# Optimization experiments

Hardware: AMD Instinct MI355X
Metric: run time of the kernel (lower is better)

Reference implementation:

```python
import jax, jax.numpy as jnp
import numpy as np

N_NODES = 50000
N_EDGES = 1600000
DIM = 32
N_STEPS = 10   # torchdiffeq rk4 with step_size=0.1 over t in [0, 1]
H = 0.1


def setup_inputs() -> dict:
    key = jax.random.key(0)
    ks = jax.random.split(key, 10)
    x = jax.random.normal(ks[0], (N_NODES, DIM), dtype=jnp.float32)
    pos_edge_index = jax.random.randint(ks[1], (2, N_EDGES), 0, N_NODES, dtype=jnp.int64)
    neg_edge_index = jax.random.randint(ks[2], (2, N_EDGES), 0, N_NODES, dtype=jnp.int64)
    s = 1.0 / np.sqrt(DIM)
    W_pos = jax.random.normal(ks[3], (DIM, DIM), dtype=jnp.float32) * s
    b_pos = jnp.zeros((DIM,), dtype=jnp.float32)
    wt_pos = jax.random.normal(ks[4], (DIM,), dtype=jnp.float32)
    W_neg = jax.random.normal(ks[5], (DIM, DIM), dtype=jnp.float32) * s
    b_neg = jnp.zeros((DIM,), dtype=jnp.float32)
    wt_neg = jax.random.normal(ks[6], (DIM,), dtype=jnp.float32)
    return {"x": x, "pos_edge_index": pos_edge_index, "neg_edge_index": neg_edge_index,
            "W_pos": W_pos, "b_pos": b_pos, "wt_pos": wt_pos,
            "W_neg": W_neg, "b_neg": b_neg, "wt_neg": wt_neg}


def _gcn_ode(x0, edge_index, W, b, wt):
    # PyG GCNConv with self-loops + symmetric normalization, wrapped in
    # psi(t, x) = relu(GCN(x)) * sigmoid(t * wt), integrated with RK4.
    src, dst = edge_index[0], edge_index[1]
    n = x0.shape[0]
    deg = jnp.zeros((n,), dtype=x0.dtype).at[dst].add(1.0) + 1.0  # self-loop
    dis = jax.lax.rsqrt(deg)
    edge_norm = (dis[src] * dis[dst])[:, None]   # [E,1]
    self_norm = (dis * dis)[:, None]             # [N,1] = 1/deg

    def f(t, x):
        xw = x @ W                               # [N,D]
        agg = jax.ops.segment_sum(edge_norm * xw[src], dst, num_segments=n)
        agg = agg + self_norm * xw + b
        gate = jax.nn.sigmoid(t * wt)            # [D]
        return jax.nn.relu(agg) * gate

    def step(x, t):
        k1 = f(t, x)
        k2 = f(t + H / 2, x + (H / 2) * k1)
        k3 = f(t + H / 2, x + (H / 2) * k2)
        k4 = f(t + H, x + H * k3)
        return x + (H / 6) * (k1 + 2 * k2 + 2 * k3 + k4), None

    ts = jnp.arange(N_STEPS, dtype=x0.dtype) * H
    xT, _ = jax.lax.scan(step, x0, ts)
    return xT


def reference(x, pos_edge_index, neg_edge_index, W_pos, b_pos, wt_pos, W_neg, b_neg, wt_neg):
    z_pos = _gcn_ode(x, pos_edge_index, W_pos, b_pos, wt_pos)
    z_neg = _gcn_ode(x, neg_edge_index, W_neg, b_neg, wt_neg)
    return (z_pos, z_neg)
```

## Files before the change

kernel.cpp:

```cpp
#include <hip/hip_runtime.h>

#define NN 50000
#define NE 1600000
#define DIM 32
#define HS 0.1f
#define NBPS 782
#define NEB4 1563
#define NNB 196
#define NSC 49
#define SBIN 256
#define NBIN 196
#define AB 391
#define WCAP 22528

static inline int cdiv(int a, int b) { return (a + b - 1) / b; }

typedef unsigned short ushort_t;
typedef unsigned v4u __attribute__((ext_vector_type(4)));


__device__ __forceinline__ float4 bf4_to_f4(uint2 u) {
    float4 v;
    v.x = __uint_as_float(u.x << 16);
    v.y = __uint_as_float(u.x & 0xffff0000u);
    v.z = __uint_as_float(u.y << 16);
    v.w = __uint_as_float(u.y & 0xffff0000u);
    return v;
}
__device__ __forceinline__ unsigned pack_bf2(float a, float b) {
    unsigned ua = __float_as_uint(a);
    ua = (ua + 0x7fffu + ((ua >> 16) & 1u)) >> 16;
    unsigned ub = __float_as_uint(b);
    ub = (ub + 0x7fffu + ((ub >> 16) & 1u)) & 0xffff0000u;
    return ua | ub;
}
__device__ __forceinline__ uint4 pack_bf8(float4 a, float4 b) {
    return make_uint4(pack_bf2(a.x, a.y), pack_bf2(a.z, a.w),
                      pack_bf2(b.x, b.y), pack_bf2(b.z, b.w));
}


__global__ void k_zero2(int* __restrict__ p0, int* __restrict__ p1) {
    int b = blockIdx.x, sg = b & 1;
    int i = (b >> 1) * 256 + (int)threadIdx.x;
    int* p = sg ? p1 : p0;
    if (i < NN) p[i] = 0;
}

__global__ void k_zbins(int* __restrict__ bins) {
    bins[blockIdx.x * 256 + threadIdx.x] = 0;
}

__global__ void k_hist4(const int* __restrict__ dst, int* __restrict__ cnt) {
    int base = (blockIdx.x * 256 + (int)threadIdx.x) * 4;
    if (base < NE) {
        v4u d = *(const v4u*)(dst + base);
        atomicAdd(&cnt[d.x], 1);
        atomicAdd(&cnt[d.y], 1);
        atomicAdd(&cnt[d.z], 1);
        atomicAdd(&cnt[d.w], 1);
    }
}

__global__ void k_dhist2(const int* __restrict__ c0,
                         const int* __restrict__ c1, int* __restrict__ bins) {
    __shared__ int lb[256];
    int b = blockIdx.x, sg = b & 1;
    int t = threadIdx.x;
    lb[t] = 0;
    __syncthreads();
    int n = (b >> 1) * 256 + t;
    if (n < NN) {
        const int* cnt = sg ? c1 : c0;
        int d = cnt[n]; if (d > 255) d = 255;
        atomicAdd(&lb[d], 1);
    }
    __syncthreads();
    int v = lb[t];
    if (v) atomicAdd(&bins[sg * 256 + t], v);
}

__global__ void k_dscan(int* __restrict__ bins) {
    __shared__ int s[256];
    int sg = blockIdx.x, t = threadIdx.x;
    s[t] = bins[sg * 256 + (255 - t)];
    __syncthreads();
    for (int off = 1; off < 256; off <<= 1) {
        int a = (t >= off) ? s[t - off] : 0;
        __syncthreads();
        s[t] += a;
        __syncthreads();
    }
    int ex = (t == 0) ? 0 : s[t - 1];
    bins[sg * 256 + (255 - t)] = ex;
}

__global__ void k_dperm2(const int* __restrict__ c0,
                         const int* __restrict__ c1, int* __restrict__ bins,
                         int* __restrict__ perm0, int* __restrict__ perm1,
                         int* __restrict__ pos0, int* __restrict__ pos1,
                         float* __restrict__ q0, float* __restrict__ q1) {
    __shared__ int lb[256];
    int b = blockIdx.x, sg = b & 1;
    int t = threadIdx.x;
    lb[t] = 0;
    __syncthreads();
    int n = (b >> 1) * 256 + t;
    const int* cnt = sg ? c1 : c0;
    int d = 0, lr = 0;
    if (n < NN) {
        d = cnt[n]; if (d > 255) d = 255;
        lr = atomicAdd(&lb[d], 1);
    }
    __syncthreads();
    int v = lb[t];
    __syncthreads();
    int base = 0;
    if (v) base = atomicAdd(&bins[sg * 256 + t], v);
    lb[t] = base;
    __syncthreads();
    if (n < NN) {
        int p = lb[d] + lr;
        int* perm = sg ? perm1 : perm0;
        int* pos  = sg ? pos1 : pos0;
        float* dq = sg ? q1 : q0;
        perm[p] = n;
        pos[n] = p;
        dq[p] = rsqrtf((float)cnt[n] + 1.0f);
    }
}

__global__ __launch_bounds__(1024) void k_scanA2(const int* __restrict__ c0,
                                                 const int* __restrict__ c1,
                                                 const int* __restrict__ perm0,
                                                 const int* __restrict__ perm1,
                                                 int* __restrict__ r0,
                                                 int* __restrict__ r1,
                                                 int* __restrict__ p0,
                                                 int* __restrict__ p1) {
    int sg = blockIdx.x >= NSC;
    int bb = blockIdx.x - (sg ? NSC : 0);
    const int* cnt  = sg ? c1 : c0;
    const int* perm = sg ? perm1 : perm0;
    int* row_ptr    = sg ? r1 : r0;
    int* partials   = sg ? p1 : p0;
    __shared__ int s[1024];
    int t = threadIdx.x;
    int g = bb * 1024 + t;
    int v = (g < NN) ? ((cnt[perm[g]] + 7) & ~7) : 0;
    s[t] = v;
    __syncthreads();
    for (int off = 1; off < 1024; off <<= 1) {
        int add = (t >= off) ? s[t - off] : 0;
        __syncthreads();
        s[t] += add;
        __syncthreads();
    }
    if (g < NN) row_ptr[g + 1] = s[t];
    if (t == 1023) partials[bb] = s[t];
}

__global__ void k_scanB2(int* __restrict__ p0, int* __restrict__ p1) {
    int* partials = blockIdx.x ? p1 : p0;
    if (threadIdx.x == 0) {
        int run = 0;
        for (int i = 0; i < NSC; i++) { int v = partials[i]; partials[i] = run; run += v; }
    }
}

__global__ void k_scanC2(int* __restrict__ r0, int* __restrict__ r1,
                         const int* __restrict__ p0, const int* __restrict__ p1) {
    int b = blockIdx.x, sg = b & 1;
    int g = (b >> 1) * 256 + (int)threadIdx.x;
    int* row_ptr = sg ? r1 : r0;
    const int* partials = sg ? p1 : p0;
    if (g < NN) row_ptr[g + 1] += partials[g >> 10];
    if (g == 0) row_ptr[0] = 0;
}


__global__ __launch_bounds__(512) void k_countA(const int* __restrict__ d0,
                        const int* __restrict__ d1,
                        const int* __restrict__ pos0, const int* __restrict__ pos1,
                        int* __restrict__ gc0, int* __restrict__ gc1) {
    __shared__ int lc[NBIN];
    int b = blockIdx.x, sg = b & 1, blk = b >> 1;
    int t = threadIdx.x;
    if (t < NBIN) lc[t] = 0;
    __syncthreads();
    const int* dst = sg ? d1 : d0;
    const int* pos = sg ? pos1 : pos0;
#pragma unroll
    for (int i = 0; i < 8; i++) {
        int e = blk * 4096 + i * 512 + t;
        if (e < NE) atomicAdd(&lc[pos[dst[e]] >> 8], 1);
    }
    __syncthreads();
    int* gc = sg ? gc1 : gc0;
    if (t < NBIN) gc[blk * NBIN + t] = lc[t];
}

__global__ __launch_bounds__(512) void k_scanM1(int* __restrict__ gc0,
                                                int* __restrict__ gc1,
                                                int* __restrict__ bint) {
    __shared__ int s[512];
    int b = blockIdx.x, sg = b & 1, bin = b >> 1;
    int* gc = sg ? gc1 : gc0;
    int t = threadIdx.x;
    int v = (t < AB) ? gc[t * NBIN + bin] : 0;
    s[t] = v;
    __syncthreads();
    for (int off = 1; off < 512; off <<= 1) {
        int a = (t >= off) ? s[t - off] : 0;
        __syncthreads();
        s[t] += a;
        __syncthreads();
    }
    if (t < AB) gc[t * NBIN + bin] = s[t] - v;
    if (t == AB - 1) bint[sg * NBIN + bin] = s[t];
}

__global__ __launch_bounds__(256) void k_scanM2(const int* __restrict__ bint,
                                                int* __restrict__ binbase) {
    __shared__ int s[256];
    int t = threadIdx.x;
    for (int sg = 0; sg < 2; sg++) {
        int v = (t < NBIN) ? bint[sg * NBIN + t] : 0;
        s[t] = v;
        __syncthreads();
        for (int off = 1; off < 256; off <<= 1) {
            int a = (t >= off) ? s[t - off] : 0;
            __syncthreads();
            s[t] += a;
            __syncthreads();
        }
        if (t < NBIN) binbase[sg * NBIN + t] = s[t] - v;
        __syncthreads();
    }
}

__global__ __launch_bounds__(512) void k_scatA(const int* __restrict__ s0s,
                        const int* __restrict__ s0d,
                        const int* __restrict__ s1s, const int* __restrict__ s1d,
                        const int* __restrict__ pos0, const int* __restrict__ pos1,
                        const int* __restrict__ gc0, const int* __restrict__ gc1,
                        const int* __restrict__ binbase,
                        unsigned* __restrict__ gst0, unsigned* __restrict__ gst1) {
    __shared__ int lc[NBIN];
    __shared__ int lst[NBIN];
    __shared__ int gch[NBIN];
    __shared__ unsigned stag[4096];
    __shared__ ushort_t bos[4096];
    int b = blockIdx.x, sg = b & 1, blk = b >> 1;
    int t = threadIdx.x;
    if (t < NBIN) lc[t] = 0;
    __syncthreads();
    const int* src = sg ? s1s : s0s;
    const int* dst = sg ? s1d : s0d;
    const int* pos = sg ? pos1 : pos0;
    const int* gc  = sg ? gc1 : gc0;
    unsigned er[8]; int ebin[8]; int erk[8];
#pragma unroll
    for (int i = 0; i < 8; i++) {
        int e = blk * 4096 + i * 512 + t;
        ebin[i] = -1;
        if (e < NE) {
            int pd = pos[dst[e]];
            int ps = pos[src[e]];
            int bin = pd >> 8;
            ebin[i] = bin;
            er[i] = ((unsigned)ps << 8) | (unsigned)(pd & 255);
            erk[i] = atomicAdd(&lc[bin], 1);
        }
    }
    __syncthreads();
    if (t < NBIN) lst[t] = lc[t];
    __syncthreads();
    for (int off = 1; off < NBIN; off <<= 1) {
        int a = (t >= off && t < NBIN) ? lst[t - off] : 0;
        __syncthreads();
        if (t < NBIN) lst[t] += a;
        __syncthreads();
    }
    if (t < NBIN) {
        lst[t] -= lc[t];
        gch[t] = binbase[sg * NBIN + t] + gc[blk * NBIN + t];
    }
    __syncthreads();
#pragma unroll
    for (int i = 0; i < 8; i++) {
        if (ebin[i] >= 0) {
            int slot = lst[ebin[i]] + erk[i];
            stag[slot] = er[i];
            bos[slot] = (ushort_t)ebin[i];
        }
    }
    __syncthreads();
    unsigned* gst = sg ? gst1 : gst0;
    int tot = (blk * 4096 + 4096 <= NE) ? 4096 : (NE - blk * 4096);
#pragma unroll
    for (int i = 0; i < 8; i++) {
        int slot = i * 512 + t;
        if (slot < tot) {
            int bin = bos[slot];
            gst[gch[bin] + (slot - lst[bin])] = stag[slot];
        }
    }
}

__global__ __launch_bounds__(512) void k_scatB(const int* __restrict__ r0,
                        const int* __restrict__ r1,
                        const unsigned* __restrict__ gst0,
                        const unsigned* __restrict__ gst1,
                        const int* __restrict__ bint, const int* __restrict__ binbase,
                        ushort_t* __restrict__ w0, ushort_t* __restrict__ w1) {
    __shared__ uint4 winq[WCAP / 8];
    __shared__ int lrp[SBIN + 1];
    __shared__ int lfill[SBIN];
    ushort_t* win = (ushort_t*)winq;
    int b = blockIdx.x, sg = b & 1, bin = b >> 1;
    int t = threadIdx.x;
    const int* rp = sg ? r1 : r0;
    const unsigned* gst = sg ? gst1 : gst0;
    ushort_t* cw = sg ? w1 : w0;
    int p0 = bin * SBIN;
    int nn = NN - p0; if (nn > SBIN) nn = SBIN;
    if (t <= nn) lrp[t] = rp[p0 + t];
    if (t < nn) lfill[t] = 0;
    __syncthreads();
    int wb = lrp[0];
    int wl = lrp[nn] - wb;
    int cnt = bint[sg * NBIN + bin];
    int base = binbase[sg * NBIN + bin];
    if (wl <= WCAP) {
        for (int i = t; i < cnt; i += 512) {
            unsigned e = gst[base + i];
            int pdl = e & 255u;
            int ofs = atomicAdd(&lfill[pdl], 1);
            win[lrp[pdl] - wb + ofs] = (ushort_t)(e >> 8);
        }
        __syncthreads();
        for (int ln = t; ln < nn; ln += 512) {
            int e0 = lrp[ln] - wb + lfill[ln], e1 = lrp[ln + 1] - wb;
            for (int j = e0; j < e1; j++) win[j] = (ushort_t)NN;
        }
        __syncthreads();
        uint4* dst4 = (uint4*)(cw + wb);
        int nq = wl >> 3;
        for (int i = t; i < nq; i += 512) dst4[i] = winq[i];
    } else {
        for (int i = t; i < cnt; i += 512) {
            unsigned e = gst[base + i];
            int pdl = e & 255u;
            int ofs = atomicAdd(&lfill[pdl], 1);
            cw[lrp[pdl] + ofs] = (ushort_t)(e >> 8);
        }
        __syncthreads();
        for (int ln = t; ln < nn; ln += 512) {
            int e0 = lrp[ln] + lfill[ln], e1 = lrp[ln + 1];
            for (int j = e0; j < e1; j++) cw[j] = (ushort_t)NN;
        }
    }
}

struct ZArgs { unsigned* p[6]; };
__global__ void k_zrow(ZArgs z) {
    int t = threadIdx.x;
    if (t < 96) z.p[t >> 4][(size_t)NN * 16 + (t & 15)] = 0u;
}

__global__ __launch_bounds__(256) void k_matmul(const float* __restrict__ src,
                                                const float* __restrict__ W,
                                                const int* __restrict__ cnt,
                                                const int* __restrict__ pos,
                                                uint2* __restrict__ xw,
                                                float* __restrict__ copy_out) {
    __shared__ float sW[DIM * DIM];
    __shared__ float sX[32 * 33];
    int t = threadIdx.x;
#pragma unroll
    for (int k = 0; k < 4; k++) { int i = k * 256 + t; sW[i] = W[i]; }
    size_t base = (size_t)blockIdx.x * 32 * DIM;
#pragma unroll
    for (int k = 0; k < 4; k++) {
        int i = k * 256 + t;
        size_t g = base + i;
        float v = 0.f;
        if (g < (size_t)NN * DIM) {
            v = src[g];
            copy_out[g] = v;
        }
        sX[(i >> 5) * 33 + (i & 31)] = v;
    }
    __syncthreads();
    int r = t >> 3, oct = t & 7;
    int row = blockIdx.x * 32 + r;
    if (row >= NN) return;
    float a0 = 0.f, a1 = 0.f, a2 = 0.f, a3 = 0.f;
    const float* xr = &sX[r * 33];
#pragma unroll
    for (int i = 0; i < DIM; i++) {
        float xv = xr[i];
        const float* wr = &sW[i * DIM + oct * 4];
        a0 = fmaf(xv, wr[0], a0);
        a1 = fmaf(xv, wr[1], a1);
        a2 = fmaf(xv, wr[2], a2);
        a3 = fmaf(xv, wr[3], a3);
    }
    float dn = rsqrtf((float)cnt[row] + 1.0f);
    a0 *= dn; a1 *= dn; a2 *= dn; a3 *= dn;
    xw[(size_t)pos[row] * 8 + oct] = make_uint2(pack_bf2(a0, a1), pack_bf2(a2, a3));
}


struct SignP {
    const int* row_ptr; const ushort_t* cw; const float* dis;
    const int* perm;
    const uint4* xw_in; uint4* xw_out; const uint4* xw_base;
    uint4* acc;
    float* x_cur;
    const float* W; const float* b; const float* wt;
    float* zout;
};
struct StageArgs { SignP s[2]; float t, stage_coef; int mode; };

#define EDGE_ADD(u)                                                     \
    {                                                                   \
        float4 vA = bf4_to_f4(make_uint2((u).x, (u).y));                \
        float4 vB = bf4_to_f4(make_uint2((u).z, (u).w));                \
        sum0.x += vA.x; sum0.y += vA.y; sum0.z += vA.z; sum0.w += vA.w; \
        sum1.x += vB.x; sum1.y += vB.y; sum1.z += vB.z; sum1.w += vB.w; \
    }

__global__ __launch_bounds__(256) void k_stage(StageArgs A) {
    int sg = blockIdx.x & 1;
    int blk = blockIdx.x >> 1;
    SignP P = A.s[sg];

    __shared__ float sW[DIM * DIM];
    __shared__ float sR[64 * 36];
    int tid = threadIdx.x;
    int mode = A.mode;
    if (mode != 5) {
#pragma unroll
        for (int k = 0; k < 4; k++) { int i = k * 256 + tid; sW[i] = P.W[i]; }
    }

    int c = tid & 3;
    int nl = tid >> 2;
    int n = blk * 64 + nl;
    bool active = n < NN;
    float dn = 0.f;
    float4 r40 = make_float4(0.f, 0.f, 0.f, 0.f);
    float4 r41 = make_float4(0.f, 0.f, 0.f, 0.f);
    float4 bs0 = make_float4(0.f, 0.f, 0.f, 0.f);
    float4 bs1 = make_float4(0.f, 0.f, 0.f, 0.f);

    if (active) {
        int e = P.row_ptr[n], e1 = P.row_ptr[n + 1];
        const uint4* xwq = P.xw_in + c;
        const uint4* cw4 = (const uint4*)P.cw;
        int q = e >> 3, qe = e1 >> 3;
        float4 sum0 = make_float4(0.f, 0.f, 0.f, 0.f);
        float4 sum1 = make_float4(0.f, 0.f, 0.f, 0.f);
        uint4 ra;
        if (q < qe) ra = cw4[q];
        while (q < qe) {
            unsigned s0 = ra.x & 0xffffu, s1 = ra.x >> 16;
            unsigned s2 = ra.y & 0xffffu, s3 = ra.y >> 16;
            unsigned s4 = ra.z & 0xffffu, s5 = ra.z >> 16;
            unsigned s6 = ra.w & 0xffffu, s7 = ra.w >> 16;
            uint4 u0 = xwq[(size_t)s0 * 4];
            uint4 u1 = xwq[(size_t)s1 * 4];
            uint4 u2 = xwq[(size_t)s2 * 4];
            uint4 u3 = xwq[(size_t)s3 * 4];
            uint4 u4 = xwq[(size_t)s4 * 4];
            uint4 u5 = xwq[(size_t)s5 * 4];
            uint4 u6 = xwq[(size_t)s6 * 4];
            uint4 u7 = xwq[(size_t)s7 * 4];
            int qn = q + 1;
            uint4 nx;
            if (qn < qe) nx = cw4[qn];
            EDGE_ADD(u0) EDGE_ADD(u1) EDGE_ADD(u2) EDGE_ADD(u3)
            EDGE_ADD(u4) EDGE_ADD(u5) EDGE_ADD(u6) EDGE_ADD(u7)
            if (qn < qe) ra = nx;
            q = qn;
        }
        dn = P.dis[n];
        uint4 un = xwq[(size_t)n * 4];
        float4 vn0 = bf4_to_f4(make_uint2(un.x, un.y));
        float4 vn1 = bf4_to_f4(make_uint2(un.z, un.w));
        float4 bb0 = *(const float4*)&P.b[c * 8];
        float4 bb1 = *(const float4*)&P.b[c * 8 + 4];
        sum0.x = fmaf(dn, sum0.x + vn0.x, bb0.x);
        sum0.y = fmaf(dn, sum0.y + vn0.y, bb0.y);
        sum0.z = fmaf(dn, sum0.z + vn0.z, bb0.z);
        sum0.w = fmaf(dn, sum0.w + vn0.w, bb0.w);
        sum1.x = fmaf(dn, sum1.x + vn1.x, bb1.x);
        sum1.y = fmaf(dn, sum1.y + vn1.y, bb1.y);
        sum1.z = fmaf(dn, sum1.z + vn1.z, bb1.z);
        sum1.w = fmaf(dn, sum1.w + vn1.w, bb1.w);
        float4 w40 = *(const float4*)&P.wt[c * 8];
        float4 w41 = *(const float4*)&P.wt[c * 8 + 4];
        float t = A.t;
        float4 kv0, kv1;
        kv0.x = fmaxf(sum0.x, 0.f) / (1.f + __expf(-t * w40.x));
        kv0.y = fmaxf(sum0.y, 0.f) / (1.f + __expf(-t * w40.y));
        kv0.z = fmaxf(sum0.z, 0.f) / (1.f + __expf(-t * w40.z));
        kv0.w = fmaxf(sum0.w, 0.f) / (1.f + __expf(-t * w40.w));
        kv1.x = fmaxf(sum1.x, 0.f) / (1.f + __expf(-t * w41.x));
        kv1.y = fmaxf(sum1.y, 0.f) / (1.f + __expf(-t * w41.y));
        kv1.z = fmaxf(sum1.z, 0.f) / (1.f + __expf(-t * w41.z));
        kv1.w = fmaxf(sum1.w, 0.f) / (1.f + __expf(-t * w41.w));

        uint4* accp = P.acc + (size_t)n * 4 + c;
        if (mode == 1) {
            *accp = pack_bf8(kv0, kv1);
            r40 = kv0; r41 = kv1;
            bs0 = vn0; bs1 = vn1;
        } else if (mode <= 3) {
            uint4 ao = *accp;
            float4 a0 = bf4_to_f4(make_uint2(ao.x, ao.y));
            float4 a1 = bf4_to_f4(make_uint2(ao.z, ao.w));
            a0.x = fmaf(2.f, kv0.x, a0.x); a0.y = fmaf(2.f, kv0.y, a0.y);
            a0.z = fmaf(2.f, kv0.z, a0.z); a0.w = fmaf(2.f, kv0.w, a0.w);
            a1.x = fmaf(2.f, kv1.x, a1.x); a1.y = fmaf(2.f, kv1.y, a1.y);
            a1.z = fmaf(2.f, kv1.z, a1.z); a1.w = fmaf(2.f, kv1.w, a1.w);
            *accp = pack_bf8(a0, a1);
            r40 = kv0; r41 = kv1;
            uint4 ub = P.xw_base[(size_t)n * 4 + c];
            bs0 = bf4_to_f4(make_uint2(ub.x, ub.y));
            bs1 = bf4_to_f4(make_uint2(ub.z, ub.w));
        } else {
            uint4 ao = *accp;
            float4 f0 = bf4_to_f4(make_uint2(ao.x, ao.y));
            float4 f1 = bf4_to_f4(make_uint2(ao.z, ao.w));
            f0.x += kv0.x; f0.y += kv0.y; f0.z += kv0.z; f0.w += kv0.w;
            f1.x += kv1.x; f1.y += kv1.y; f1.z += kv1.z; f1.w += kv1.w;
            int id = P.perm[n];
            size_t o = (size_t)id * DIM + c * 8;
            float4 xc0 = *(const float4*)&P.x_cur[o];
            float4 xc1 = *(const float4*)&P.x_cur[o + 4];
            float4 xn0, xn1;
            xn0.x = fmaf(HS / 6.f, f0.x, xc0.x); xn0.y = fmaf(HS / 6.f, f0.y, xc0.y);
            xn0.z = fmaf(HS / 6.f, f0.z, xc0.z); xn0.w = fmaf(HS / 6.f, f0.w, xc0.w);
            xn1.x = fmaf(HS / 6.f, f1.x, xc1.x); xn1.y = fmaf(HS / 6.f, f1.y, xc1.y);
            xn1.z = fmaf(HS / 6.f, f1.z, xc1.z); xn1.w = fmaf(HS / 6.f, f1.w, xc1.w);
            if (mode == 4) {
                *(float4*)&P.x_cur[o] = xn0;
                *(float4*)&P.x_cur[o + 4] = xn1;
                r40 = f0; r41 = f1;
                uint4 ub = P.xw_base[(size_t)n * 4 + c];
                bs0 = bf4_to_f4(make_uint2(ub.x, ub.y));
                bs1 = bf4_to_f4(make_uint2(ub.z, ub.w));
            } else {
                *(float4*)&P.zout[o] = xn0;
                *(float4*)&P.zout[o + 4] = xn1;
            }
        }
    }

    if (mode == 5) return;

    *(float4*)&sR[nl * 36 + c * 8] = r40;
    *(float4*)&sR[nl * 36 + c * 8 + 4] = r41;
    __syncthreads();
    if (active) {
        float4 y0 = make_float4(0.f, 0.f, 0.f, 0.f);
        float4 y1 = make_float4(0.f, 0.f, 0.f, 0.f);
        const float* row = &sR[nl * 36];
#pragma unroll
        for (int i = 0; i < DIM; i++) {
            float sv = row[i];
            float4 wA = *(const float4*)&sW[i * DIM + c * 8];
            float4 wB = *(const float4*)&sW[i * DIM + c * 8 + 4];
            y0.x = fmaf(sv, wA.x, y0.x); y0.y = fmaf(sv, wA.y, y0.y);
            y0.z = fmaf(sv, wA.z, y0.z); y0.w = fmaf(sv, wA.w, y0.w);
            y1.x = fmaf(sv, wB.x, y1.x); y1.y = fmaf(sv, wB.y, y1.y);
            y1.z = fmaf(sv, wB.z, y1.z); y1.w = fmaf(sv, wB.w, y1.w);
        }
        float sd = A.stage_coef * dn;
        y0.x = fmaf(sd, y0.x, bs0.x); y0.y = fmaf(sd, y0.y, bs0.y);
        y0.z = fmaf(sd, y0.z, bs0.z); y0.w = fmaf(sd, y0.w, bs0.w);
        y1.x = fmaf(sd, y1.x, bs1.x); y1.y = fmaf(sd, y1.y, bs1.y);
        y1.z = fmaf(sd, y1.z, bs1.z); y1.w = fmaf(sd, y1.w, bs1.w);
        P.xw_out[(size_t)n * 4 + c] = pack_bf8(y0, y1);
    }
}


extern "C" void kernel_launch(void* const* d_in, const int* in_sizes, int n_in,
                              void* d_out, int out_size, void* d_ws, size_t ws_size,
                              hipStream_t stream) {
    const float* x   = (const float*)d_in[0];
    const int* epos  = (const int*)d_in[1];
    const int* eneg  = (const int*)d_in[2];
    const float* Wp  = (const float*)d_in[3];
    const float* bp  = (const float*)d_in[4];
    const float* wtp = (const float*)d_in[5];
    const float* Wn  = (const float*)d_in[6];
    const float* bn  = (const float*)d_in[7];
    const float* wtn = (const float*)d_in[8];
    float* out = (float*)d_out;

    char* ws = (char*)d_ws;
    size_t off = 0;
    auto alloc = [&](size_t bytes) -> void* {
        void* p = ws + off;
        off += (bytes + 255) & ~(size_t)255;
        return p;
    };

    struct Sign {
        int *row_ptr, *cnt, *partials, *perm, *pos, *gcnt;
        unsigned* gstage;
        float* dis;
        ushort_t* cw;
        float* x_cur;
        uint4* acc;
        uint4* xwbuf[3];
        const int *src, *dst;
        const float *W, *b, *wt;
        float* zout;
    } S[2];

    const size_t CWCAP = (size_t)NE + 8u * NN;
    int* dbins   = (int*)alloc(2 * 256 * sizeof(int));
    int* bint    = (int*)alloc(2 * NBIN * sizeof(int));
    int* binbase = (int*)alloc(2 * NBIN * sizeof(int));

    for (int s = 0; s < 2; s++) {
        S[s].row_ptr  = (int*)alloc((NN + 1) * sizeof(int));
        S[s].cnt      = (int*)alloc(NN * sizeof(int));
        S[s].partials = (int*)alloc(256);
        S[s].perm     = (int*)alloc(NN * sizeof(int));
        S[s].pos      = (int*)alloc(NN * sizeof(int));
        S[s].gcnt     = (int*)alloc((size_t)AB * NBIN * sizeof(int));
        S[s].gstage   = (unsigned*)alloc((size_t)NE * sizeof(unsigned));
        S[s].dis      = (float*)alloc(NN * sizeof(float));
        S[s].cw       = (ushort_t*)alloc(CWCAP * sizeof(ushort_t));
        S[s].x_cur    = (float*)alloc((size_t)NN * DIM * sizeof(float));
        S[s].acc      = (uint4*)alloc((size_t)NN * DIM * 2);
        S[s].xwbuf[0] = (uint4*)alloc((size_t)(NN + 1) * DIM * 2);
        S[s].xwbuf[1] = (uint4*)alloc((size_t)(NN + 1) * DIM * 2);
        S[s].xwbuf[2] = (uint4*)alloc((size_t)(NN + 1) * DIM * 2);
    }
    S[0].src = epos; S[0].dst = epos + NE; S[0].W = Wp; S[0].b = bp; S[0].wt = wtp;
    S[0].zout = out;
    S[1].src = eneg; S[1].dst = eneg + NE; S[1].W = Wn; S[1].b = bn; S[1].wt = wtn;
    S[1].zout = out + (size_t)NN * DIM;

    k_zero2<<<2 * NNB, 256, 0, stream>>>(S[0].cnt, S[1].cnt);
    k_zbins<<<2, 256, 0, stream>>>(dbins);
    for (int s = 0; s < 2; s++)
        k_hist4<<<NEB4, 256, 0, stream>>>(S[s].dst, S[s].cnt);
    k_dhist2<<<2 * NNB, 256, 0, stream>>>(S[0].cnt, S[1].cnt, dbins);
    k_dscan<<<2, 256, 0, stream>>>(dbins);
    k_dperm2<<<2 * NNB, 256, 0, stream>>>(S[0].cnt, S[1].cnt, dbins,
                                          S[0].perm, S[1].perm, S[0].pos, S[1].pos,
                                          S[0].dis, S[1].dis);
    k_scanA2<<<2 * NSC, 1024, 0, stream>>>(S[0].cnt, S[1].cnt, S[0].perm, S[1].perm,
                                           S[0].row_ptr, S[1].row_ptr,
                                           S[0].partials, S[1].partials);
    k_scanB2<<<2, 1, 0, stream>>>(S[0].partials, S[1].partials);
    k_scanC2<<<2 * NNB, 256, 0, stream>>>(S[0].row_ptr, S[1].row_ptr,
                                          S[0].partials, S[1].partials);
    k_countA<<<2 * AB, 512, 0, stream>>>(S[0].dst, S[1].dst, S[0].pos, S[1].pos,
                                         S[0].gcnt, S[1].gcnt);
    k_scanM1<<<2 * NBIN, 512, 0, stream>>>(S[0].gcnt, S[1].gcnt, bint);
    k_scanM2<<<1, 256, 0, stream>>>(bint, binbase);
    k_scatA<<<2 * AB, 512, 0, stream>>>(S[0].src, S[0].dst, S[1].src, S[1].dst,
                                        S[0].pos, S[1].pos, S[0].gcnt, S[1].gcnt,
                                        binbase, S[0].gstage, S[1].gstage);
    k_scatB<<<2 * NBIN, 512, 0, stream>>>(S[0].row_ptr, S[1].row_ptr,
                                          S[0].gstage, S[1].gstage,
                                          bint, binbase, S[0].cw, S[1].cw);

    ZArgs Z;
    for (int s = 0; s < 2; s++)
        for (int k = 0; k < 3; k++) Z.p[s * 3 + k] = (unsigned*)S[s].xwbuf[k];
    k_zrow<<<1, 96, 0, stream>>>(Z);
    for (int s = 0; s < 2; s++)
        k_matmul<<<cdiv(NN, 32), 256, 0, stream>>>(x, S[s].W, S[s].cnt, S[s].pos,
                                                   (uint2*)S[s].xwbuf[0], S[s].x_cur);

    for (int st = 0; st < 10; st++) {
        float tb = HS * (float)st;
        struct Ph { float t, sc; int mode, in, out; } ph[4] = {
            { tb,             HS * 0.5f, 1,              0, 1 },
            { tb + HS * 0.5f, HS * 0.5f, 2,              1, 2 },
            { tb + HS * 0.5f, HS,        3,              2, 1 },
            { tb + HS,        HS / 6.f,  st == 9 ? 5 : 4, 1, 0 },
        };
        for (int p = 0; p < 4; p++) {
            StageArgs A;
            for (int s = 0; s < 2; s++) {
                A.s[s].row_ptr = S[s].row_ptr;
                A.s[s].cw      = S[s].cw;
                A.s[s].dis     = S[s].dis;
                A.s[s].perm    = S[s].perm;
                A.s[s].xw_in   = S[s].xwbuf[ph[p].in];
                A.s[s].xw_out  = S[s].xwbuf[ph[p].out];
                A.s[s].xw_base = S[s].xwbuf[0];
                A.s[s].acc     = S[s].acc;
                A.s[s].x_cur   = S[s].x_cur;
                A.s[s].W       = S[s].W;
                A.s[s].b       = S[s].b;
                A.s[s].wt      = S[s].wt;
                A.s[s].zout    = S[s].zout;
            }
            A.t = ph[p].t; A.stage_coef = ph[p].sc; A.mode = ph[p].mode;
            k_stage<<<2 * NBPS, 256, 0, stream>>>(A);
        }
    }
}
```

Baseline: 1.382 ms.

## Compute degrees and per-bin degree sort from staged edges, drop global histogram passes

Edges are now bucketed by original destination index, and a new per-bin kernel counts degrees from the staged edges, sorts nodes by degree within each 256-node bin and builds row pointers. This replaces the global atomic histogram, the global degree sort and the multi-kernel scan chain, which removes several launches and one full pass of edge atomics. The cost is a degree sort that is only local to each bin rather than global, which may change load balance in the aggregation kernels. It also adds a pos[] gather for source indices in the final scatter.

```diff
diff --git a/kernel.cpp b/kernel.cpp
--- a/kernel.cpp
+++ b/kernel.cpp
@@ -5,9 +5,7 @@
 #define DIM 32
 #define HS 0.1f
 #define NBPS 782
-#define NEB4 1563
 #define NNB 196
-#define NSC 49
 #define SBIN 256
 #define NBIN 196
 #define AB 391
@@ -16,7 +14,6 @@
 static inline int cdiv(int a, int b) { return (a + b - 1) / b; }
 
 typedef unsigned short ushort_t;
-typedef unsigned v4u __attribute__((ext_vector_type(4)));
 
 
 __device__ __forceinline__ float4 bf4_to_f4(uint2 u) {
@@ -40,148 +37,8 @@
 }
 
 
-__global__ void k_zero2(int* __restrict__ p0, int* __restrict__ p1) {
-    int b = blockIdx.x, sg = b & 1;
-    int i = (b >> 1) * 256 + (int)threadIdx.x;
-    int* p = sg ? p1 : p0;
-    if (i < NN) p[i] = 0;
-}
-
-__global__ void k_zbins(int* __restrict__ bins) {
-    bins[blockIdx.x * 256 + threadIdx.x] = 0;
-}
-
-__global__ void k_hist4(const int* __restrict__ dst, int* __restrict__ cnt) {
-    int base = (blockIdx.x * 256 + (int)threadIdx.x) * 4;
-    if (base < NE) {
-        v4u d = *(const v4u*)(dst + base);
-        atomicAdd(&cnt[d.x], 1);
-        atomicAdd(&cnt[d.y], 1);
-        atomicAdd(&cnt[d.z], 1);
-        atomicAdd(&cnt[d.w], 1);
-    }
-}
-
-__global__ void k_dhist2(const int* __restrict__ c0,
-                         const int* __restrict__ c1, int* __restrict__ bins) {
-    __shared__ int lb[256];
-    int b = blockIdx.x, sg = b & 1;
-    int t = threadIdx.x;
-    lb[t] = 0;
-    __syncthreads();
-    int n = (b >> 1) * 256 + t;
-    if (n < NN) {
-        const int* cnt = sg ? c1 : c0;
-        int d = cnt[n]; if (d > 255) d = 255;
-        atomicAdd(&lb[d], 1);
-    }
-    __syncthreads();
-    int v = lb[t];
-    if (v) atomicAdd(&bins[sg * 256 + t], v);
-}
-
-__global__ void k_dscan(int* __restrict__ bins) {
-    __shared__ int s[256];
-    int sg = blockIdx.x, t = threadIdx.x;
-    s[t] = bins[sg * 256 + (255 - t)];
-    __syncthreads();
-    for (int off = 1; off < 256; off <<= 1) {
-        int a = (t >= off) ? s[t - off] : 0;
-        __syncthreads();
-        s[t] += a;
-        __syncthreads();
-    }
-    int ex = (t == 0) ? 0 : s[t - 1];
-    bins[sg * 256 + (255 - t)] = ex;
-}
-
-__global__ void k_dperm2(const int* __restrict__ c0,
-                         const int* __restrict__ c1, int* __restrict__ bins,
-                         int* __restrict__ perm0, int* __restrict__ perm1,
-                         int* __restrict__ pos0, int* __restrict__ pos1,
-                         float* __restrict__ q0, float* __restrict__ q1) {
-    __shared__ int lb[256];
-    int b = blockIdx.x, sg = b & 1;
-    int t = threadIdx.x;
-    lb[t] = 0;
-    __syncthreads();
-    int n = (b >> 1) * 256 + t;
-    const int* cnt = sg ? c1 : c0;
-    int d = 0, lr = 0;
-    if (n < NN) {
-        d = cnt[n]; if (d > 255) d = 255;
-        lr = atomicAdd(&lb[d], 1);
-    }
-    __syncthreads();
-    int v = lb[t];
-    __syncthreads();
-    int base = 0;
-    if (v) base = atomicAdd(&bins[sg * 256 + t], v);
-    lb[t] = base;
-    __syncthreads();
-    if (n < NN) {
-        int p = lb[d] + lr;
-        int* perm = sg ? perm1 : perm0;
-        int* pos  = sg ? pos1 : pos0;
-        float* dq = sg ? q1 : q0;
-        perm[p] = n;
-        pos[n] = p;
-        dq[p] = rsqrtf((float)cnt[n] + 1.0f);
-    }
-}
-
-__global__ __launch_bounds__(1024) void k_scanA2(const int* __restrict__ c0,
-                                                 const int* __restrict__ c1,
-                                                 const int* __restrict__ perm0,
-                                                 const int* __restrict__ perm1,
-                                                 int* __restrict__ r0,
-                                                 int* __restrict__ r1,
-                                                 int* __restrict__ p0,
-                                                 int* __restrict__ p1) {
-    int sg = blockIdx.x >= NSC;
-    int bb = blockIdx.x - (sg ? NSC : 0);
-    const int* cnt  = sg ? c1 : c0;
-    const int* perm = sg ? perm1 : perm0;
-    int* row_ptr    = sg ? r1 : r0;
-    int* partials   = sg ? p1 : p0;
-    __shared__ int s[1024];
-    int t = threadIdx.x;
-    int g = bb * 1024 + t;
-    int v = (g < NN) ? ((cnt[perm[g]] + 7) & ~7) : 0;
-    s[t] = v;
-    __syncthreads();
-    for (int off = 1; off < 1024; off <<= 1) {
-        int add = (t >= off) ? s[t - off] : 0;
-        __syncthreads();
-        s[t] += add;
-        __syncthreads();
-    }
-    if (g < NN) row_ptr[g + 1] = s[t];
-    if (t == 1023) partials[bb] = s[t];
-}
-
-__global__ void k_scanB2(int* __restrict__ p0, int* __restrict__ p1) {
-    int* partials = blockIdx.x ? p1 : p0;
-    if (threadIdx.x == 0) {
-        int run = 0;
-        for (int i = 0; i < NSC; i++) { int v = partials[i]; partials[i] = run; run += v; }
-    }
-}
-
-__global__ void k_scanC2(int* __restrict__ r0, int* __restrict__ r1,
-                         const int* __restrict__ p0, const int* __restrict__ p1) {
-    int b = blockIdx.x, sg = b & 1;
-    int g = (b >> 1) * 256 + (int)threadIdx.x;
-    int* row_ptr = sg ? r1 : r0;
-    const int* partials = sg ? p1 : p0;
-    if (g < NN) row_ptr[g + 1] += partials[g >> 10];
-    if (g == 0) row_ptr[0] = 0;
-}
-
-
 __global__ __launch_bounds__(512) void k_countA(const int* __restrict__ d0,
                         const int* __restrict__ d1,
-                        const int* __restrict__ pos0, const int* __restrict__ pos1,
                         int* __restrict__ gc0, int* __restrict__ gc1) {
     __shared__ int lc[NBIN];
     int b = blockIdx.x, sg = b & 1, blk = b >> 1;
@@ -189,11 +46,10 @@
     if (t < NBIN) lc[t] = 0;
     __syncthreads();
     const int* dst = sg ? d1 : d0;
-    const int* pos = sg ? pos1 : pos0;
 #pragma unroll
     for (int i = 0; i < 8; i++) {
         int e = blk * 4096 + i * 512 + t;
-        if (e < NE) atomicAdd(&lc[pos[dst[e]] >> 8], 1);
+        if (e < NE) atomicAdd(&lc[dst[e] >> 8], 1);
     }
     __syncthreads();
     int* gc = sg ? gc1 : gc0;
@@ -242,7 +98,6 @@
 __global__ __launch_bounds__(512) void k_scatA(const int* __restrict__ s0s,
                         const int* __restrict__ s0d,
                         const int* __restrict__ s1s, const int* __restrict__ s1d,
-                        const int* __restrict__ pos0, const int* __restrict__ pos1,
                         const int* __restrict__ gc0, const int* __restrict__ gc1,
                         const int* __restrict__ binbase,
                         unsigned* __restrict__ gst0, unsigned* __restrict__ gst1) {
@@ -257,7 +112,6 @@
     __syncthreads();
     const int* src = sg ? s1s : s0s;
     const int* dst = sg ? s1d : s0d;
-    const int* pos = sg ? pos1 : pos0;
     const int* gc  = sg ? gc1 : gc0;
     unsigned er[8]; int ebin[8]; int erk[8];
 #pragma unroll
@@ -265,11 +119,10 @@
         int e = blk * 4096 + i * 512 + t;
         ebin[i] = -1;
         if (e < NE) {
-            int pd = pos[dst[e]];
-            int ps = pos[src[e]];
-            int bin = pd >> 8;
+            int d = dst[e];
+            int bin = d >> 8;
             ebin[i] = bin;
-            er[i] = ((unsigned)ps << 8) | (unsigned)(pd & 255);
+            er[i] = ((unsigned)src[e] << 8) | (unsigned)(d & 255);
             erk[i] = atomicAdd(&lc[bin], 1);
         }
     }
@@ -308,25 +161,127 @@
     }
 }
 
+__global__ __launch_bounds__(256) void k_degB(
+        const unsigned* __restrict__ gst0, const unsigned* __restrict__ gst1,
+        const int* __restrict__ bint, const int* __restrict__ binbase,
+        int* __restrict__ c0, int* __restrict__ c1,
+        int* __restrict__ pos0, int* __restrict__ pos1,
+        int* __restrict__ perm0, int* __restrict__ perm1,
+        float* __restrict__ q0, float* __restrict__ q1,
+        int* __restrict__ r0, int* __restrict__ r1,
+        int* __restrict__ bt0, int* __restrict__ bt1) {
+    __shared__ int deg[SBIN];
+    __shared__ int dh[256];
+    __shared__ int spd[SBIN];
+    __shared__ int s[256];
+    int b = blockIdx.x, sg = b & 1, bin = b >> 1;
+    int t = threadIdx.x;
+    const unsigned* gst = sg ? gst1 : gst0;
+    int p0 = bin * SBIN;
+    int nn = NN - p0; if (nn > SBIN) nn = SBIN;
+    deg[t] = 0; dh[t] = 0;
+    __syncthreads();
+    int cntr = bint[sg * NBIN + bin];
+    int base = binbase[sg * NBIN + bin];
+    for (int i = t; i < cntr; i += 256)
+        atomicAdd(&deg[gst[base + i] & 255u], 1);
+    __syncthreads();
+    int d = 0, dc = 0;
+    if (t < nn) {
+        d = deg[t];
+        dc = d > 255 ? 255 : d;
+        atomicAdd(&dh[dc], 1);
+    }
+    __syncthreads();
+    s[t] = dh[255 - t];
+    __syncthreads();
+    for (int off = 1; off < 256; off <<= 1) {
+        int a = (t >= off) ? s[t - off] : 0;
+        __syncthreads();
+        s[t] += a;
+        __syncthreads();
+    }
+    int ex = (t == 0) ? 0 : s[t - 1];
+    __syncthreads();
+    dh[255 - t] = ex;
+    __syncthreads();
+    if (t < nn) {
+        int r = atomicAdd(&dh[dc], 1);
+        int* cnt = sg ? c1 : c0;
+        int* pos = sg ? pos1 : pos0;
+        int* perm = sg ? perm1 : perm0;
+        float* dq = sg ? q1 : q0;
+        cnt[p0 + t] = d;
+        pos[p0 + t] = p0 + r;
+        perm[p0 + r] = p0 + t;
+        dq[p0 + r] = rsqrtf((float)d + 1.0f);
+        spd[r] = (d + 7) & ~7;
+    }
+    __syncthreads();
+    int v = (t < nn) ? spd[t] : 0;
+    s[t] = v;
+    __syncthreads();
+    for (int off = 1; off < 256; off <<= 1) {
+        int a = (t >= off) ? s[t - off] : 0;
+        __syncthreads();
+        s[t] += a;
+        __syncthreads();
+    }
+    int* rp = sg ? r1 : r0;
+    int* bt = sg ? bt1 : bt0;
+    if (t < nn) rp[p0 + t + 1] = s[t];
+    if (t == nn - 1) bt[bin] = s[t];
+}
+
+__global__ __launch_bounds__(256) void k_binscan(int* __restrict__ bt0,
+                                                 int* __restrict__ bt1) {
+    __shared__ int s[256];
+    int sg = blockIdx.x, t = threadIdx.x;
+    int* bt = sg ? bt1 : bt0;
+    int v = (t < NBIN) ? bt[t] : 0;
+    s[t] = v;
+    __syncthreads();
+    for (int off = 1; off < 256; off <<= 1) {
+        int a = (t >= off) ? s[t - off] : 0;
+        __syncthreads();
+        s[t] += a;
+        __syncthreads();
+    }
+    if (t < NBIN) bt[t] = s[t] - v;
+}
+
+__global__ void k_rowfix(int* __restrict__ r0, int* __restrict__ r1,
+                         const int* __restrict__ bt0, const int* __restrict__ bt1) {
+    int b = blockIdx.x, sg = b & 1;
+    int g = (b >> 1) * 256 + (int)threadIdx.x;
+    int* rp = sg ? r1 : r0;
+    const int* bt = sg ? bt1 : bt0;
+    if (g < NN) rp[g + 1] += bt[g >> 8];
+    if (g == 0) rp[0] = 0;
+}
+
 __global__ __launch_bounds__(512) void k_scatB(const int* __restrict__ r0,
                         const int* __restrict__ r1,
                         const unsigned* __restrict__ gst0,
                         const unsigned* __restrict__ gst1,
                         const int* __restrict__ bint, const int* __restrict__ binbase,
+                        const int* __restrict__ pos0, const int* __restrict__ pos1,
                         ushort_t* __restrict__ w0, ushort_t* __restrict__ w1) {
     __shared__ uint4 winq[WCAP / 8];
     __shared__ int lrp[SBIN + 1];
     __shared__ int lfill[SBIN];
+    __shared__ int lpos[SBIN];
     ushort_t* win = (ushort_t*)winq;
     int b = blockIdx.x, sg = b & 1, bin = b >> 1;
     int t = threadIdx.x;
     const int* rp = sg ? r1 : r0;
     const unsigned* gst = sg ? gst1 : gst0;
+    const int* pos = sg ? pos1 : pos0;
     ushort_t* cw = sg ? w1 : w0;
     int p0 = bin * SBIN;
     int nn = NN - p0; if (nn > SBIN) nn = SBIN;
     if (t <= nn) lrp[t] = rp[p0 + t];
-    if (t < nn) lfill[t] = 0;
+    if (t < nn) { lfill[t] = 0; lpos[t] = pos[p0 + t] - p0; }
     __syncthreads();
     int wb = lrp[0];
     int wl = lrp[nn] - wb;
@@ -335,9 +290,10 @@
     if (wl <= WCAP) {
         for (int i = t; i < cnt; i += 512) {
             unsigned e = gst[base + i];
-            int pdl = e & 255u;
-            int ofs = atomicAdd(&lfill[pdl], 1);
-            win[lrp[pdl] - wb + ofs] = (ushort_t)(e >> 8);
+            int rl = lpos[e & 255u];
+            int ps = pos[e >> 8];
+            int ofs = atomicAdd(&lfill[rl], 1);
+            win[lrp[rl] - wb + ofs] = (ushort_t)ps;
         }
         __syncthreads();
         for (int ln = t; ln < nn; ln += 512) {
@@ -351,9 +307,10 @@
     } else {
         for (int i = t; i < cnt; i += 512) {
             unsigned e = gst[base + i];
-            int pdl = e & 255u;
-            int ofs = atomicAdd(&lfill[pdl], 1);
-            cw[lrp[pdl] + ofs] = (ushort_t)(e >> 8);
+            int rl = lpos[e & 255u];
+            int ps = pos[e >> 8];
+            int ofs = atomicAdd(&lfill[rl], 1);
+            cw[lrp[rl] + ofs] = (ushort_t)ps;
         }
         __syncthreads();
         for (int ln = t; ln < nn; ln += 512) {
@@ -612,7 +569,7 @@
     };
 
     struct Sign {
-        int *row_ptr, *cnt, *partials, *perm, *pos, *gcnt;
+        int *row_ptr, *cnt, *perm, *pos, *gcnt, *btot;
         unsigned* gstage;
         float* dis;
         ushort_t* cw;
@@ -625,17 +582,16 @@
     } S[2];
 
     const size_t CWCAP = (size_t)NE + 8u * NN;
-    int* dbins   = (int*)alloc(2 * 256 * sizeof(int));
     int* bint    = (int*)alloc(2 * NBIN * sizeof(int));
     int* binbase = (int*)alloc(2 * NBIN * sizeof(int));
 
     for (int s = 0; s < 2; s++) {
         S[s].row_ptr  = (int*)alloc((NN + 1) * sizeof(int));
         S[s].cnt      = (int*)alloc(NN * sizeof(int));
-        S[s].partials = (int*)alloc(256);
         S[s].perm     = (int*)alloc(NN * sizeof(int));
         S[s].pos      = (int*)alloc(NN * sizeof(int));
         S[s].gcnt     = (int*)alloc((size_t)AB * NBIN * sizeof(int));
+        S[s].btot     = (int*)alloc(NBIN * sizeof(int));
         S[s].gstage   = (unsigned*)alloc((size_t)NE * sizeof(unsigned));
         S[s].dis      = (float*)alloc(NN * sizeof(float));
         S[s].cw       = (ushort_t*)alloc(CWCAP * sizeof(ushort_t));
@@ -650,31 +606,24 @@
     S[1].src = eneg; S[1].dst = eneg + NE; S[1].W = Wn; S[1].b = bn; S[1].wt = wtn;
     S[1].zout = out + (size_t)NN * DIM;
 
-    k_zero2<<<2 * NNB, 256, 0, stream>>>(S[0].cnt, S[1].cnt);
-    k_zbins<<<2, 256, 0, stream>>>(dbins);
-    for (int s = 0; s < 2; s++)
-        k_hist4<<<NEB4, 256, 0, stream>>>(S[s].dst, S[s].cnt);
-    k_dhist2<<<2 * NNB, 256, 0, stream>>>(S[0].cnt, S[1].cnt, dbins);
-    k_dscan<<<2, 256, 0, stream>>>(dbins);
-    k_dperm2<<<2 * NNB, 256, 0, stream>>>(S[0].cnt, S[1].cnt, dbins,
-                                          S[0].perm, S[1].perm, S[0].pos, S[1].pos,
-                                          S[0].dis, S[1].dis);
-    k_scanA2<<<2 * NSC, 1024, 0, stream>>>(S[0].cnt, S[1].cnt, S[0].perm, S[1].perm,
-                                           S[0].row_ptr, S[1].row_ptr,
-                                           S[0].partials, S[1].partials);
-    k_scanB2<<<2, 1, 0, stream>>>(S[0].partials, S[1].partials);
-    k_scanC2<<<2 * NNB, 256, 0, stream>>>(S[0].row_ptr, S[1].row_ptr,
-                                          S[0].partials, S[1].partials);
-    k_countA<<<2 * AB, 512, 0, stream>>>(S[0].dst, S[1].dst, S[0].pos, S[1].pos,
-                                         S[0].gcnt, S[1].gcnt);
+    k_countA<<<2 * AB, 512, 0, stream>>>(S[0].dst, S[1].dst, S[0].gcnt, S[1].gcnt);
     k_scanM1<<<2 * NBIN, 512, 0, stream>>>(S[0].gcnt, S[1].gcnt, bint);
     k_scanM2<<<1, 256, 0, stream>>>(bint, binbase);
     k_scatA<<<2 * AB, 512, 0, stream>>>(S[0].src, S[0].dst, S[1].src, S[1].dst,
-                                        S[0].pos, S[1].pos, S[0].gcnt, S[1].gcnt,
-                                        binbase, S[0].gstage, S[1].gstage);
+                                        S[0].gcnt, S[1].gcnt, binbase,
+                                        S[0].gstage, S[1].gstage);
+    k_degB<<<2 * NBIN, 256, 0, stream>>>(S[0].gstage, S[1].gstage, bint, binbase,
+                                         S[0].cnt, S[1].cnt, S[0].pos, S[1].pos,
+                                         S[0].perm, S[1].perm, S[0].dis, S[1].dis,
+                                         S[0].row_ptr, S[1].row_ptr,
+                                         S[0].btot, S[1].btot);
+    k_binscan<<<2, 256, 0, stream>>>(S[0].btot, S[1].btot);
+    k_rowfix<<<2 * NNB, 256, 0, stream>>>(S[0].row_ptr, S[1].row_ptr,
+                                          S[0].btot, S[1].btot);
     k_scatB<<<2 * NBIN, 512, 0, stream>>>(S[0].row_ptr, S[1].row_ptr,
                                           S[0].gstage, S[1].gstage,
-                                          bint, binbase, S[0].cw, S[1].cw);
+                                          bint, binbase, S[0].pos, S[1].pos,
+                                          S[0].cw, S[1].cw);
 
     ZArgs Z;
     for (int s = 0; s < 2; s++)
```

Result: no change. 1.389 ms (+0.5%).
